# Performance work log

Measured on AMD Instinct MI355X. Metric: run time of the kernel, lower is better.

The kernel has to match this reference:

```python
import jax, jax.numpy as jnp
import numpy as np
import math

N_HEAD = 16

def setup_inputs() -> dict:
    key = jax.random.key(0)
    k1, k2, k3 = jax.random.split(key, 3)
    B, T, C = 4, 2048, 1024
    x = jax.random.normal(k1, (B, T, C), dtype=jnp.float32)
    W_attn = jax.random.normal(k2, (C, 3 * C), dtype=jnp.float32) * 0.02
    b_attn = jnp.zeros((3 * C,), dtype=jnp.float32)
    W_proj = jax.random.normal(k3, (C, C), dtype=jnp.float32) * 0.02
    b_proj = jnp.zeros((C,), dtype=jnp.float32)
    return {"x": x, "W_attn": W_attn, "b_attn": b_attn, "W_proj": W_proj, "b_proj": b_proj}

def reference(x, W_attn, b_attn, W_proj, b_proj):
    B, T, C = x.shape
    H = N_HEAD
    hd = C // H
    qkv = x @ W_attn + b_attn                      # [B,T,3C]
    # Faithful to source bug: q, k, v ALL built from the k-slice of qkv.
    k_slice = qkv[:, :, C:2 * C]
    k = k_slice.reshape(B, T, H, hd).transpose(0, 2, 1, 3)  # [B,H,T,hd]
    q = k
    v = k
    att = jnp.einsum('bhqd,bhkd->bhqk', q, k) / math.sqrt(hd)  # [B,H,T,T]
    causal = jnp.tril(jnp.ones((T, T), dtype=bool))
    att = jnp.where(causal[None, None], att, jnp.finfo(att.dtype).min)
    att = jax.nn.softmax(att, axis=-1)
    y = jnp.einsum('bhqk,bhkd->bhqd', att, v)      # [B,H,T,hd]
    y = y.transpose(0, 2, 1, 3).reshape(B, T, C)
    return y @ W_proj + b_proj
```

## Files before the change

kernel.cpp:

```cpp
#include <hip/hip_runtime.h>

#define T_SEQ 2048
#define C_DIM 1024
#define HD 64

typedef __attribute__((ext_vector_type(8))) short short8;
typedef __attribute__((ext_vector_type(4))) float f32x4;
typedef __attribute__((ext_vector_type(4))) unsigned int uint4v;

extern "C" __device__ float __ocml_native_exp2_f32(float);

__device__ __forceinline__ unsigned short f2bf(float f) {
  unsigned int u = __builtin_bit_cast(unsigned int, f);
  u += 0x7fffu + ((u >> 16) & 1u);
  return (unsigned short)(u >> 16);
}

__device__ __forceinline__ unsigned cvt_pk_bf16(float lo, float hi) {
  unsigned r;
  asm("v_cvt_pk_bf16_f32 %0, %1, %2" : "=v"(r) : "v"(lo), "v"(hi));
  return r;
}

__global__ __launch_bounds__(256) void transpose_w(
    const float* __restrict__ src, unsigned short* __restrict__ dst,
    int src_ld, int col_off) {
  int n = blockIdx.x * 16 + threadIdx.x;
  int k = blockIdx.y * 16 + threadIdx.y;
  dst[(size_t)n * C_DIM + k] = f2bf(src[(size_t)k * src_ld + col_off + n]);
}

__global__ __launch_bounds__(256) void gemm_xw(
    const float* __restrict__ A, const unsigned short* __restrict__ Bt,
    const float* __restrict__ bias, unsigned short* __restrict__ out,
    unsigned short* __restrict__ vt) {
  __shared__ unsigned short Als[128][40];
  __shared__ unsigned short Bls[128][40];
  const int tid = threadIdx.x;
  const int l = tid & 63, w = tid >> 6;
  const int wr = w >> 1, wc = w & 1;
  const int rb = blockIdx.x * 128, cb = blockIdx.y * 128;
  const int srow = tid >> 1, sh = (tid & 1) * 16;
  f32x4 acc[4][4] = {};
  for (int kb = 0; kb < 1024; kb += 32) {
    const f32x4* ap = (const f32x4*)(A + (size_t)(rb + srow) * 1024 + kb + sh);
    f32x4 a0 = ap[0], a1 = ap[1], a2 = ap[2], a3 = ap[3];
    short8 s0, s1;
#pragma unroll
    for (int i = 0; i < 4; ++i) {
      s0[i]     = (short)f2bf(a0[i]);
      s0[i + 4] = (short)f2bf(a1[i]);
      s1[i]     = (short)f2bf(a2[i]);
      s1[i + 4] = (short)f2bf(a3[i]);
    }
    *(short8*)&Als[srow][sh] = s0;
    *(short8*)&Als[srow][sh + 8] = s1;
    const short8* bp = (const short8*)(Bt + (size_t)(cb + srow) * 1024 + kb + sh);
    short8 b0 = bp[0], b1 = bp[1];
    *(short8*)&Bls[srow][sh] = b0;
    *(short8*)&Bls[srow][sh + 8] = b1;
    __syncthreads();
    short8 af[4], bfr[4];
#pragma unroll
    for (int m = 0; m < 4; ++m)
      af[m] = *(const short8*)&Als[wr * 64 + m * 16 + (l & 15)][(l >> 4) * 8];
#pragma unroll
    for (int n = 0; n < 4; ++n)
      bfr[n] = *(const short8*)&Bls[wc * 64 + n * 16 + (l & 15)][(l >> 4) * 8];
#pragma unroll
    for (int m = 0; m < 4; ++m)
#pragma unroll
      for (int n = 0; n < 4; ++n)
        acc[m][n] = __builtin_amdgcn_mfma_f32_16x16x32_bf16(af[m], bfr[n], acc[m][n], 0, 0, 0);
    __syncthreads();
  }
  const int rg = (l >> 4) * 4, cg = l & 15;
#pragma unroll
  for (int m = 0; m < 4; ++m)
#pragma unroll
    for (int n = 0; n < 4; ++n) {
      int col = cb + wc * 64 + n * 16 + cg;
      float bv = bias[col];
      int row0 = rb + wr * 64 + m * 16 + rg;
      unsigned short e0 = f2bf(acc[m][n][0] + bv);
      unsigned short e1 = f2bf(acc[m][n][1] + bv);
      unsigned short e2 = f2bf(acc[m][n][2] + bv);
      unsigned short e3 = f2bf(acc[m][n][3] + bv);
      size_t bhd = (size_t)((row0 >> 11) * 16 + (col >> 6));
      size_t kidx = (bhd * T_SEQ + (row0 & 2047)) * HD + (col & 63);
      out[kidx]          = e0;
      out[kidx + HD]     = e1;
      out[kidx + 2 * HD] = e2;
      out[kidx + 3 * HD] = e3;
      unsigned long long pv = (unsigned long long)e0 | ((unsigned long long)e1 << 16)
                            | ((unsigned long long)e2 << 32) | ((unsigned long long)e3 << 48);
      *(unsigned long long*)&vt[(bhd * HD + (col & 63)) * T_SEQ + (row0 & 2047)] = pv;
    }
}

__global__ __launch_bounds__(256) void gemm_yw(
    const unsigned short* __restrict__ A, const unsigned short* __restrict__ Bt,
    const float* __restrict__ bias, float* __restrict__ out) {
  __shared__ unsigned short Als[128][40];
  __shared__ unsigned short Bls[128][40];
  const int tid = threadIdx.x;
  const int l = tid & 63, w = tid >> 6;
  const int wr = w >> 1, wc = w & 1;
  const int rb = blockIdx.x * 128, cb = blockIdx.y * 128;
  const int srow = tid >> 1, sh = (tid & 1) * 16;
  f32x4 acc[4][4] = {};
  for (int kb = 0; kb < 1024; kb += 32) {
    const short8* ap = (const short8*)(A + (size_t)(rb + srow) * 1024 + kb + sh);
    short8 a0 = ap[0], a1 = ap[1];
    *(short8*)&Als[srow][sh] = a0;
    *(short8*)&Als[srow][sh + 8] = a1;
    const short8* bp = (const short8*)(Bt + (size_t)(cb + srow) * 1024 + kb + sh);
    short8 b0 = bp[0], b1 = bp[1];
    *(short8*)&Bls[srow][sh] = b0;
    *(short8*)&Bls[srow][sh + 8] = b1;
    __syncthreads();
    short8 af[4], bfr[4];
#pragma unroll
    for (int m = 0; m < 4; ++m)
      af[m] = *(const short8*)&Als[wr * 64 + m * 16 + (l & 15)][(l >> 4) * 8];
#pragma unroll
    for (int n = 0; n < 4; ++n)
      bfr[n] = *(const short8*)&Bls[wc * 64 + n * 16 + (l & 15)][(l >> 4) * 8];
#pragma unroll
    for (int m = 0; m < 4; ++m)
#pragma unroll
      for (int n = 0; n < 4; ++n)
        acc[m][n] = __builtin_amdgcn_mfma_f32_16x16x32_bf16(af[m], bfr[n], acc[m][n], 0, 0, 0);
    __syncthreads();
  }
  const int rg = (l >> 4) * 4, cg = l & 15;
#pragma unroll
  for (int m = 0; m < 4; ++m)
#pragma unroll
    for (int n = 0; n < 4; ++n) {
      int col = cb + wc * 64 + n * 16 + cg;
      float bv = bias[col];
#pragma unroll
      for (int r = 0; r < 4; ++r) {
        int row = rb + wr * 64 + m * 16 + rg + r;
        out[(size_t)row * 1024 + col] = acc[m][n][r] + bv;
      }
    }
}

__device__ __forceinline__ void sm_group(
    f32x4 (&s)[4], int qq, int kvb, bool needmask, int g,
    float& mrun, float& lrun, f32x4 (&yacc)[4],
    int src01, int src23, bool hi2, short8 (&pa)[2]) {
  if (needmask) {
    const int lim = qq - kvb;
#pragma unroll
    for (int b = 0; b < 4; ++b)
#pragma unroll
      for (int r = 0; r < 4; ++r)
        if (16 * b + 4 * g + r > lim) s[b][r] = -INFINITY;
  }
  float mt = fmaxf(fmaxf(s[0][0], s[0][1]), fmaxf(s[0][2], s[0][3]));
#pragma unroll
  for (int b = 1; b < 4; ++b)
    mt = fmaxf(mt, fmaxf(fmaxf(s[b][0], s[b][1]), fmaxf(s[b][2], s[b][3])));
  mt = fmaxf(mt, __shfl_xor(mt, 16));
  mt = fmaxf(mt, __shfl_xor(mt, 32));
  if (!__all(mt <= mrun + 11.5416f)) {
    float mn = fmaxf(mrun, mt);
    float al = __ocml_native_exp2_f32(mrun - mn);
    mrun = mn;
    lrun *= al;
    float a0 = __shfl(al, 4 * g + 0);
    float a1 = __shfl(al, 4 * g + 1);
    float a2 = __shfl(al, 4 * g + 2);
    float a3 = __shfl(al, 4 * g + 3);
#pragma unroll
    for (int nb = 0; nb < 4; ++nb) {
      yacc[nb][0] *= a0; yacc[nb][1] *= a1;
      yacc[nb][2] *= a2; yacc[nb][3] *= a3;
    }
  }
  float ps = 0.f;
  unsigned pk[4][2];
#pragma unroll
  for (int b = 0; b < 4; ++b) {
    float p0 = __ocml_native_exp2_f32(s[b][0] - mrun);
    float p1 = __ocml_native_exp2_f32(s[b][1] - mrun);
    float p2 = __ocml_native_exp2_f32(s[b][2] - mrun);
    float p3 = __ocml_native_exp2_f32(s[b][3] - mrun);
    ps += (p0 + p1) + (p2 + p3);
    pk[b][0] = cvt_pk_bf16(p0, p1);
    pk[b][1] = cvt_pk_bf16(p2, p3);
  }
  ps += __shfl_xor(ps, 16);
  ps += __shfl_xor(ps, 32);
  lrun += ps;
  {
    unsigned x0a = (unsigned)__shfl((int)pk[0][0], src01);
    unsigned x1a = (unsigned)__shfl((int)pk[1][0], src01);
    unsigned x0b = (unsigned)__shfl((int)pk[0][1], src01);
    unsigned x1b = (unsigned)__shfl((int)pk[1][1], src01);
    unsigned y0a = (unsigned)__shfl((int)pk[0][0], src23);
    unsigned y1a = (unsigned)__shfl((int)pk[1][0], src23);
    unsigned y0b = (unsigned)__shfl((int)pk[0][1], src23);
    unsigned y1b = (unsigned)__shfl((int)pk[1][1], src23);
    uint4v u;
    u.x = hi2 ? x1a : x0a;
    u.y = hi2 ? x1b : x0b;
    u.z = hi2 ? y1a : y0a;
    u.w = hi2 ? y1b : y0b;
    pa[0] = __builtin_bit_cast(short8, u);
  }
  {
    unsigned x0a = (unsigned)__shfl((int)pk[2][0], src01);
    unsigned x1a = (unsigned)__shfl((int)pk[3][0], src01);
    unsigned x0b = (unsigned)__shfl((int)pk[2][1], src01);
    unsigned x1b = (unsigned)__shfl((int)pk[3][1], src01);
    unsigned y0a = (unsigned)__shfl((int)pk[2][0], src23);
    unsigned y1a = (unsigned)__shfl((int)pk[3][0], src23);
    unsigned y0b = (unsigned)__shfl((int)pk[2][1], src23);
    unsigned y1b = (unsigned)__shfl((int)pk[3][1], src23);
    uint4v u;
    u.x = hi2 ? x1a : x0a;
    u.y = hi2 ? x1b : x0b;
    u.z = hi2 ? y1a : y0a;
    u.w = hi2 ? y1b : y0b;
    pa[1] = __builtin_bit_cast(short8, u);
  }
}

__global__ __launch_bounds__(64, 4) void attn_fwd(
    const unsigned short* __restrict__ Khb, const unsigned short* __restrict__ Vt,
    unsigned short* __restrict__ Y) {
  const int id = blockIdx.x;
  const int bh = id & 63;
  const int chunk = 63 - (id >> 6);
  const int l = threadIdx.x & 63;
  const int i = l & 15, g = l >> 4;
  const unsigned short* kbase = Khb + (size_t)bh * T_SEQ * HD;
  const unsigned short* vbase = Vt + (size_t)bh * HD * T_SEQ;

  const int q0 = chunk * 32;
  const int qA = q0 + i, qB = q0 + 16 + i;

  short8 qa0 = *(const short8*)(kbase + (size_t)qA * HD + g * 8);
  short8 qa1 = *(const short8*)(kbase + (size_t)qA * HD + 32 + g * 8);
  short8 qb0 = *(const short8*)(kbase + (size_t)qB * HD + g * 8);
  short8 qb1 = *(const short8*)(kbase + (size_t)qB * HD + 32 + g * 8);

  f32x4 ya[4] = {}, yb[4] = {};
  float mA = -INFINITY, lA = 0.f, mB = -INFINITY, lB = 0.f;

  const int nt = (q0 + 31) / 64 + 1;
  const int src01 = i + ((g & 1) << 5);
  const int src23 = src01 + 16;
  const bool hi2 = (g >> 1) != 0;
  const float SCL = 0.18033688f;

  for (int t = 0; t < nt; ++t) {
    const int kvb = t * 64;
    f32x4 sa[4], sb[4];
#pragma unroll
    for (int b = 0; b < 4; ++b) {
      const unsigned short* kp = kbase + (size_t)(kvb + 16 * b + i) * HD + g * 8;
      short8 k0 = *(const short8*)kp;
      short8 k1 = *(const short8*)(kp + 32);
      f32x4 acc = {};
      acc = __builtin_amdgcn_mfma_f32_16x16x32_bf16(k0, qa0, acc, 0, 0, 0);
      acc = __builtin_amdgcn_mfma_f32_16x16x32_bf16(k1, qa1, acc, 0, 0, 0);
      sa[b] = acc;
      f32x4 acc2 = {};
      acc2 = __builtin_amdgcn_mfma_f32_16x16x32_bf16(k0, qb0, acc2, 0, 0, 0);
      acc2 = __builtin_amdgcn_mfma_f32_16x16x32_bf16(k1, qb1, acc2, 0, 0, 0);
      sb[b] = acc2;
    }
#pragma unroll
    for (int b = 0; b < 4; ++b)
#pragma unroll
      for (int r = 0; r < 4; ++r) { sa[b][r] *= SCL; sb[b][r] *= SCL; }

    const bool needmask = (kvb + 63 > q0);
    short8 paA[2], paB[2];
    sm_group(sa, qA, kvb, needmask, g, mA, lA, ya, src01, src23, hi2, paA);
    sm_group(sb, qB, kvb, needmask, g, mB, lB, yb, src01, src23, hi2, paB);

#pragma unroll
    for (int c = 0; c < 2; ++c)
#pragma unroll
      for (int nb = 0; nb < 4; ++nb) {
        short8 vf = *(const short8*)(vbase + (size_t)(nb * 16 + i) * T_SEQ + kvb + c * 32 + g * 8);
        ya[nb] = __builtin_amdgcn_mfma_f32_16x16x32_bf16(paA[c], vf, ya[nb], 0, 0, 0);
        yb[nb] = __builtin_amdgcn_mfma_f32_16x16x32_bf16(paB[c], vf, yb[nb], 0, 0, 0);
      }
  }

  const int bb = bh >> 4, hh = bh & 15;
  float liA = 1.f / lA;
  float lA0 = __shfl(liA, 4 * g + 0);
  float lA1 = __shfl(liA, 4 * g + 1);
  float lA2 = __shfl(liA, 4 * g + 2);
  float lA3 = __shfl(liA, 4 * g + 3);
  size_t rowbase = ((size_t)bb * T_SEQ + q0 + 4 * g) * C_DIM;
#pragma unroll
  for (int nb = 0; nb < 4; ++nb) {
    int col = hh * 64 + nb * 16 + i;
    Y[rowbase + col]             = f2bf(ya[nb][0] * lA0);
    Y[rowbase + C_DIM + col]     = f2bf(ya[nb][1] * lA1);
    Y[rowbase + 2 * C_DIM + col] = f2bf(ya[nb][2] * lA2);
    Y[rowbase + 3 * C_DIM + col] = f2bf(ya[nb][3] * lA3);
  }
  float liB = 1.f / lB;
  float lB0 = __shfl(liB, 4 * g + 0);
  float lB1 = __shfl(liB, 4 * g + 1);
  float lB2 = __shfl(liB, 4 * g + 2);
  float lB3 = __shfl(liB, 4 * g + 3);
  rowbase += (size_t)16 * C_DIM;
#pragma unroll
  for (int nb = 0; nb < 4; ++nb) {
    int col = hh * 64 + nb * 16 + i;
    Y[rowbase + col]             = f2bf(yb[nb][0] * lB0);
    Y[rowbase + C_DIM + col]     = f2bf(yb[nb][1] * lB1);
    Y[rowbase + 2 * C_DIM + col] = f2bf(yb[nb][2] * lB2);
    Y[rowbase + 3 * C_DIM + col] = f2bf(yb[nb][3] * lB3);
  }
}

extern "C" void kernel_launch(void* const* d_in, const int* in_sizes, int n_in,
                              void* d_out, int out_size, void* d_ws, size_t ws_size,
                              hipStream_t stream) {
  const float* x      = (const float*)d_in[0];
  const float* W_attn = (const float*)d_in[1];
  const float* b_attn = (const float*)d_in[2];
  const float* W_proj = (const float*)d_in[3];
  const float* b_proj = (const float*)d_in[4];
  float* out = (float*)d_out;

  unsigned short* Wkt  = (unsigned short*)d_ws;
  unsigned short* Wpt  = Wkt + (size_t)1024 * 1024;
  unsigned short* Khb  = Wpt + (size_t)1024 * 1024;
  unsigned short* Ybuf = Khb + (size_t)8192 * 1024;
  unsigned short* Vtb  = Ybuf + (size_t)8192 * 1024;

  transpose_w<<<dim3(64, 64), dim3(16, 16), 0, stream>>>(W_attn, Wkt, 3072, 1024);
  transpose_w<<<dim3(64, 64), dim3(16, 16), 0, stream>>>(W_proj, Wpt, 1024, 0);

  gemm_xw<<<dim3(64, 8), 256, 0, stream>>>(x, Wkt, b_attn + 1024, Khb, Vtb);

  attn_fwd<<<dim3(4096), 64, 0, stream>>>(Khb, Vtb, Ybuf);

  gemm_yw<<<dim3(64, 8), 256, 0, stream>>>(Ybuf, Wpt, b_proj, out);
}
```

Measured before the change: 240.6 us.

## Split causal KV loop across two waves per block and merge via LDS

Each attention block now runs two waves. Each wave processes half of the KV tiles for the same 32 query rows. The second wave writes its partial output, running max and running sum to shared memory. The first wave then merges the two online-softmax states and writes the normalized bf16 output. The aim is to shorten the serial per-block KV loop and raise parallelism for the long causal rows, at the cost of a barrier, LDS traffic and a second exp/merge step.

```diff
diff --git a/kernel.cpp b/kernel.cpp
--- a/kernel.cpp
+++ b/kernel.cpp
@@ -230,19 +230,29 @@
   }
 }
 
-__global__ __launch_bounds__(64, 4) void attn_fwd(
+__global__ __launch_bounds__(128, 8) void attn_fwd(
     const unsigned short* __restrict__ Khb, const unsigned short* __restrict__ Vt,
     unsigned short* __restrict__ Y) {
   const int id = blockIdx.x;
   const int bh = id & 63;
   const int chunk = 63 - (id >> 6);
-  const int l = threadIdx.x & 63;
+  const int tid = threadIdx.x;
+  const int w = tid >> 6;
+  const int l = tid & 63;
   const int i = l & 15, g = l >> 4;
   const unsigned short* kbase = Khb + (size_t)bh * T_SEQ * HD;
   const unsigned short* vbase = Vt + (size_t)bh * HD * T_SEQ;
 
   const int q0 = chunk * 32;
   const int qA = q0 + i, qB = q0 + 16 + i;
+  const int nt = (q0 + 31) / 64 + 1;
+  const int half = (nt + 1) >> 1;
+  const int tBeg = w ? half : 0;
+  const int tEnd = w ? nt : half;
+
+  __shared__ float Ylds[32][68];
+  __shared__ float Mlds[32];
+  __shared__ float Llds[32];
 
   short8 qa0 = *(const short8*)(kbase + (size_t)qA * HD + g * 8);
   short8 qa1 = *(const short8*)(kbase + (size_t)qA * HD + 32 + g * 8);
@@ -252,13 +262,12 @@
   f32x4 ya[4] = {}, yb[4] = {};
   float mA = -INFINITY, lA = 0.f, mB = -INFINITY, lB = 0.f;
 
-  const int nt = (q0 + 31) / 64 + 1;
   const int src01 = i + ((g & 1) << 5);
   const int src23 = src01 + 16;
   const bool hi2 = (g >> 1) != 0;
   const float SCL = 0.18033688f;
 
-  for (int t = 0; t < nt; ++t) {
+  for (int t = tBeg; t < tEnd; ++t) {
     const int kvb = t * 64;
     f32x4 sa[4], sb[4];
 #pragma unroll
@@ -295,34 +304,62 @@
       }
   }
 
-  const int bb = bh >> 4, hh = bh & 15;
-  float liA = 1.f / lA;
-  float lA0 = __shfl(liA, 4 * g + 0);
-  float lA1 = __shfl(liA, 4 * g + 1);
-  float lA2 = __shfl(liA, 4 * g + 2);
-  float lA3 = __shfl(liA, 4 * g + 3);
-  size_t rowbase = ((size_t)bb * T_SEQ + q0 + 4 * g) * C_DIM;
-#pragma unroll
-  for (int nb = 0; nb < 4; ++nb) {
-    int col = hh * 64 + nb * 16 + i;
-    Y[rowbase + col]             = f2bf(ya[nb][0] * lA0);
-    Y[rowbase + C_DIM + col]     = f2bf(ya[nb][1] * lA1);
-    Y[rowbase + 2 * C_DIM + col] = f2bf(ya[nb][2] * lA2);
-    Y[rowbase + 3 * C_DIM + col] = f2bf(ya[nb][3] * lA3);
-  }
-  float liB = 1.f / lB;
-  float lB0 = __shfl(liB, 4 * g + 0);
-  float lB1 = __shfl(liB, 4 * g + 1);
-  float lB2 = __shfl(liB, 4 * g + 2);
-  float lB3 = __shfl(liB, 4 * g + 3);
-  rowbase += (size_t)16 * C_DIM;
-#pragma unroll
-  for (int nb = 0; nb < 4; ++nb) {
-    int col = hh * 64 + nb * 16 + i;
-    Y[rowbase + col]             = f2bf(yb[nb][0] * lB0);
-    Y[rowbase + C_DIM + col]     = f2bf(yb[nb][1] * lB1);
-    Y[rowbase + 2 * C_DIM + col] = f2bf(yb[nb][2] * lB2);
-    Y[rowbase + 3 * C_DIM + col] = f2bf(yb[nb][3] * lB3);
+  if (w == 1) {
+#pragma unroll
+    for (int nb = 0; nb < 4; ++nb)
+#pragma unroll
+      for (int r = 0; r < 4; ++r) {
+        Ylds[4 * g + r][nb * 16 + i]      = ya[nb][r];
+        Ylds[16 + 4 * g + r][nb * 16 + i] = yb[nb][r];
+      }
+    if (l < 16) {
+      Mlds[l]      = mA;
+      Llds[l]      = lA;
+      Mlds[16 + l] = mB;
+      Llds[16 + l] = lB;
+    }
+  }
+  __syncthreads();
+  if (w == 0) {
+    const int bb = bh >> 4, hh = bh & 15;
+    size_t rowA = ((size_t)bb * T_SEQ + q0 + 4 * g) * C_DIM;
+#pragma unroll
+    for (int r = 0; r < 4; ++r) {
+      float m0 = __shfl(mA, 4 * g + r);
+      float l0 = __shfl(lA, 4 * g + r);
+      float m1 = Mlds[4 * g + r];
+      float l1 = Llds[4 * g + r];
+      float mm = fmaxf(m0, m1);
+      float e0 = __ocml_native_exp2_f32(m0 - mm);
+      float e1 = __ocml_native_exp2_f32(m1 - mm);
+      float inv = 1.f / (l0 * e0 + l1 * e1);
+      float w0 = e0 * inv, w1 = e1 * inv;
+#pragma unroll
+      for (int nb = 0; nb < 4; ++nb) {
+        int col = hh * 64 + nb * 16 + i;
+        Y[rowA + (size_t)r * C_DIM + col] =
+            f2bf(ya[nb][r] * w0 + Ylds[4 * g + r][nb * 16 + i] * w1);
+      }
+    }
+    size_t rowB = rowA + (size_t)16 * C_DIM;
+#pragma unroll
+    for (int r = 0; r < 4; ++r) {
+      float m0 = __shfl(mB, 4 * g + r);
+      float l0 = __shfl(lB, 4 * g + r);
+      float m1 = Mlds[16 + 4 * g + r];
+      float l1 = Llds[16 + 4 * g + r];
+      float mm = fmaxf(m0, m1);
+      float e0 = __ocml_native_exp2_f32(m0 - mm);
+      float e1 = __ocml_native_exp2_f32(m1 - mm);
+      float inv = 1.f / (l0 * e0 + l1 * e1);
+      float w0 = e0 * inv, w1 = e1 * inv;
+#pragma unroll
+      for (int nb = 0; nb < 4; ++nb) {
+        int col = hh * 64 + nb * 16 + i;
+        Y[rowB + (size_t)r * C_DIM + col] =
+            f2bf(yb[nb][r] * w0 + Ylds[16 + 4 * g + r][nb * 16 + i] * w1);
+      }
+    }
   }
 }
 
@@ -347,7 +384,7 @@
 
   gemm_xw<<<dim3(64, 8), 256, 0, stream>>>(x, Wkt, b_attn + 1024, Khb, Vtb);
 
-  attn_fwd<<<dim3(4096), 64, 0, stream>>>(Khb, Vtb, Ybuf);
+  attn_fwd<<<dim3(4096), 128, 0, stream>>>(Khb, Vtb, Ybuf);
 
   gemm_yw<<<dim3(64, 8), 256, 0, stream>>>(Ybuf, Wpt, b_proj, out);
 }
```

Result: slower. 498.9 us (+107.3%).
